# Kernel tuning notes

Hardware: AMD Instinct MI355X
Metric: run time of the kernel (lower is better)

## Reference

```python
import jax, jax.numpy as jnp
import numpy as np
from jax import lax

PATCH = 15
WIDTH_DCP = 55


def _box_sum(x, r):
    # AvgPool2d(kernel=2r+1, stride=1, padding=r, count_include_pad=True) * (2r+1)^2;
    # the kernel-size factor cancels in all mean_*/N ratios below.
    return lax.reduce_window(x, 0.0, lax.add, (1, 1, 2 * r + 1, 2 * r + 1),
                             (1, 1, 1, 1), ((0, 0), (0, 0), (r, r), (r, r)))


def _guided_filter(I, p, r, eps):
    Nn = _box_sum(jnp.ones_like(p), r)
    mean_I = _box_sum(I, r) / Nn
    mean_p = _box_sum(p, r) / Nn
    mean_Ip = _box_sum(I * p, r) / Nn
    cov_Ip = mean_Ip - mean_I * mean_p
    mean_II = _box_sum(I * I, r) / Nn
    var_I = mean_II - mean_I * mean_I
    a = cov_Ip / (var_I + eps)
    b = mean_p - a * mean_I
    mean_a = _box_sum(a, r) / Nn
    mean_b = _box_sum(b, r) / Nn
    return mean_a * I + mean_b


def _dark_channel(x):
    d = x.min(axis=1, keepdims=True)
    pad = WIDTH_DCP // 2
    d = jnp.pad(d, ((0, 0), (0, 0), (pad, pad), (pad, pad)), constant_values=1.0)
    return lax.reduce_window(d, jnp.inf, lax.min, (1, 1, WIDTH_DCP, WIDTH_DCP),
                             (1, 1, 1, 1), 'VALID')


def _map_A(x):
    N, C, H, W = x.shape
    dc = _dark_channel(x).reshape(N, -1)
    k = int(H * W * 0.001)
    _, idx = lax.top_k(dc, k)  # brightest dark-channel pixels
    xr = x.reshape(N, 3, -1)
    searched = jnp.take_along_axis(xr, jnp.broadcast_to(idx[:, None, :], (N, 3, k)), axis=2)
    A = searched.mean(axis=2)
    return jnp.broadcast_to(A[:, :, None, None], x.shape)


def _t_bccr(haze, mapA, ps):
    t1 = (mapA - haze) / (mapA - 20.0 / 255.0)
    t2 = (mapA - haze) / (mapA - 300.0 / 255.0)
    t = jnp.maximum(t1, t2).max(axis=1, keepdims=True)
    pad = ps // 2
    t = jnp.pad(t, ((0, 0), (0, 0), (pad, pad), (pad, pad)), constant_values=0.0)
    t = lax.reduce_window(t, -jnp.inf, lax.max, (1, 1, ps, ps), (1, 1, 1, 1), 'VALID')
    return jnp.clip(t, 0.05, 1.0)


def _pad_reshape(data, ps):
    N, C, H, W = data.shape
    pad_H = (ps - H % ps) % ps
    pad_W = (ps - W % ps) % ps
    padded = jnp.pad(data, ((0, 0), (0, 0), (pad_H // 2, pad_H - pad_H // 2),
                            (pad_W // 2, pad_W - pad_W // 2)), mode='edge')
    nH = padded.shape[2] // ps
    nW = padded.shape[3] // ps
    p = padded[:, 0].reshape(N, nH, ps, nW, ps).transpose(0, 1, 3, 2, 4)
    p = p.reshape(N, nH * nW, ps * ps).transpose(0, 2, 1)  # [N, ps*ps, P]
    return p, pad_H // 2, pad_W // 2, nH, nW


def _transmission(S, V1, ps, pixel_number=10, slp_length=0.1):
    X, sH, sW, nH, nW = _pad_reshape(V1, ps)  # [N, pp, P]
    Y, _, _, _, _ = _pad_reshape(S, ps)
    dX = X[:, :, None, :] - X[:, None, :, :]          # [N, pp, pp, P]
    dY = Y[:, :, None, :] - Y[:, None, :, :]
    slope = dY / (dX + 1e-8)
    smask = ((slope > -1) & (slope < 0)).astype(X.dtype)
    scount = smask.sum(axis=2)                         # [N, pp, P]
    pmask = (scount >= 0.5 * ps * ps).astype(X.dtype)
    pcount = pmask.sum(axis=1, keepdims=True)          # [N, 1, P]
    mx = (X * pmask).sum(axis=1, keepdims=True) / (pcount + 1e-5)
    my = (Y * pmask).sum(axis=1, keepdims=True) / (pcount + 1e-5)
    k = ((X * Y * pmask).sum(axis=1, keepdims=True) - pcount * mx * my) / (
        ((X * pmask) ** 2).sum(axis=1, keepdims=True) - pcount * mx ** 2 + 1e-5)
    b = my - k * mx
    t = 1.0 + k / (b + 1e-8)
    length = (1.0 + k ** 2) ** 0.5 * ((X * pmask).max(axis=1, keepdims=True)
                                      - (X + 1e8 * (1.0 - pmask)).min(axis=1, keepdims=True))
    tmask = ((pcount > pixel_number) & (length > slp_length) & (k > -1) & (k < 0)
             & (t > 0.01) & (t < 1 - 0.01)).astype(X.dtype)
    t = (t * tmask).reshape(-1, 1, nH, nW)
    t = jnp.repeat(jnp.repeat(t, ps, axis=2), ps, axis=3)  # nearest upsample x ps
    return t[:, :, sH:S.shape[2] + sH, sW:S.shape[3] + sW]


def _percentile(t, bili=0.05):
    N = t.shape[0]
    flat = jnp.where(t > 0, t, 10.0).reshape(N, -1)
    s = jnp.sort(flat, axis=1)
    n = flat.shape[1]
    idx = min(int(bili * n), n - 1)
    return s[:, idx].reshape(-1, 1, 1, 1)


def _restore(image, ps=PATCH):
    mapA = _map_A(image)
    norm = image / mapA
    mx = norm.max(axis=1, keepdims=True)
    S = 1.0 - norm.min(axis=1, keepdims=True) / (mx + 1e-8)
    V1 = 1.0 / (mx + 1e-8)
    t1 = _transmission(S, V1, ps)
    half = ps // 2
    t2 = _transmission(S[:, :, half:, half:], V1[:, :, half:, half:], ps)
    t2 = jnp.pad(t2, ((0, 0), (0, 0), (half, 0), (half, 0)), constant_values=0.0)
    t_slp = jnp.where((t1 != 0) & (t2 != 0), (t1 + t2) / 2.0,
                      jnp.where(t1 != 0, t1, t2))
    t_bl = _t_bccr(image, mapA, ps)
    t_min = _percentile(t_slp)
    t_fusion = jnp.clip(jnp.where(t_slp > 0, t_slp, t_bl), t_min, 1.0)
    t_ref = _guided_filter(image.mean(axis=1, keepdims=True), t_fusion, 2 * ps, 1e-3)
    return (image - mapA) / t_ref + mapA


def setup_inputs() -> dict:
    key = jax.random.key(0)
    image = jax.random.uniform(key, (1, 3, 480, 480), dtype=jnp.float32)
    return {"image": image}


def reference(image):
    return _restore(image)
```

## Files before the change

kernel.cpp:

```cpp
#include <hip/hip_runtime.h>
#include <math.h>

#define W 480
#define HT 480
#define HW (W*HT)
#define GE (HW/256)
#define PP 225
#define NPATCH 1024
#define EQCAP 8192

struct State {
  unsigned histA[4][256];
  unsigned slotP[4];
  unsigned slotK[4];
  float sumA[3];
  unsigned eqCount;
  float A[3];
  unsigned tminbits;
  unsigned eqIdx[EQCAP];
  float tp1[NPATCH];
  float tp2[NPATCH];
};

__device__ __forceinline__ void resolve_level(const unsigned* __restrict__ h,
                                              unsigned k_in, int desc,
                                              unsigned* lds,
                                              unsigned& chosen, unsigned& k_out) {
  int t = threadIdx.x;
  unsigned c = h[desc ? (255 - t) : t];
  lds[t] = c;
  __syncthreads();
  for (int s = 1; s < 256; s <<= 1) {
    unsigned add = (t >= s) ? lds[t - s] : 0u;
    __syncthreads();
    lds[t] += add;
    __syncthreads();
  }
  unsigned incl = lds[t];
  unsigned excl = incl - c;
  if (incl >= k_in && excl < k_in) { lds[256] = (unsigned)t; lds[257] = k_in - excl; }
  __syncthreads();
  unsigned tt = lds[256];
  k_out = lds[257];
  chosen = desc ? (255u - tt) : tt;
  __syncthreads();
}

__global__ __launch_bounds__(512) void k_rowmin(const float* __restrict__ img,
                                                float* __restrict__ rowmin, State* st) {
  __shared__ float l[534];
  int y = blockIdx.x, t = threadIdx.x;
  for (int i = t; i < 534; i += 512) {
    int col = i - 27;
    float v = 1.0f;
    if ((unsigned)col < (unsigned)W) {
      int q = y * W + col;
      v = fminf(fminf(img[q], img[HW + q]), img[2 * HW + q]);
    }
    l[i] = v;
  }
  if (y == 0 && t < 256) {
    for (int i = 0; i < 4; ++i) st->histA[i][t] = 0u;
    if (t == 0) { st->sumA[0] = 0.f; st->sumA[1] = 0.f; st->sumA[2] = 0.f; st->eqCount = 0u; }
  }
  __syncthreads();
  if (t < W) {
    float m = l[t];
    for (int d = 1; d < 55; ++d) m = fminf(m, l[t + d]);
    rowmin[y * W + t] = m;
  }
}

__global__ __launch_bounds__(256) void k_vchunk(const float* __restrict__ rowmin,
                                                float* __restrict__ cmin) {
  int p = blockIdx.x * 256 + threadIdx.x;
  if (p >= 60 * W) return;
  int c = p / W, x = p - c * W;
  float m = INFINITY;
  for (int r = 0; r < 8; ++r) m = fminf(m, rowmin[(c * 8 + r) * W + x]);
  cmin[p] = m;
}

__global__ __launch_bounds__(256) void k_minV2(const float* __restrict__ rowmin,
                                               const float* __restrict__ cmin,
                                               float* __restrict__ dc, State* st) {
  __shared__ unsigned lh[256];
  int t = threadIdx.x;
  lh[t] = 0u;
  __syncthreads();
  int p = blockIdx.x * 256 + t;
  int y = p / W, x = p - y * W;
  int lo = y - 27, hi = y + 27;
  float m = (lo < 0 || hi >= HT) ? 1.0f : INFINITY;
  int lo2 = max(lo, 0), hi2 = min(hi, HT - 1);
  int cs = (lo2 + 7) >> 3, ce = ((hi2 + 1) >> 3) - 1;
  for (int c = cs; c <= ce; ++c) m = fminf(m, cmin[c * W + x]);
  for (int yy = lo2; yy < (cs << 3); ++yy) m = fminf(m, rowmin[yy * W + x]);
  for (int yy = (ce + 1) << 3; yy <= hi2; ++yy) m = fminf(m, rowmin[yy * W + x]);
  dc[p] = m;
  atomicAdd(&lh[__float_as_uint(m) >> 24], 1u);
  __syncthreads();
  unsigned c = lh[t];
  if (c) atomicAdd(&st->histA[0][t], c);
}

__global__ __launch_bounds__(256) void k_hist(const float* __restrict__ dc,
                                              State* st, int level) {
  __shared__ unsigned lds[258];
  int t = threadIdx.x;
  unsigned prefix, k;
  if (level == 1) { prefix = 0u; k = 230u; }
  else { prefix = st->slotP[level - 2]; k = st->slotK[level - 2]; }
  unsigned ch, kn;
  resolve_level(st->histA[level - 1], k, 1, lds, ch, kn);
  prefix |= ch << (32 - 8 * level);
  k = kn;
  if (t == 0) { st->slotP[level - 1] = prefix; st->slotK[level - 1] = k; }
  __syncthreads();
  lds[t] = 0u;
  __syncthreads();
  int p = blockIdx.x * 256 + t;
  unsigned bits = __float_as_uint(dc[p]);
  unsigned mask = 0xFFFFFFFFu << (32 - 8 * level);
  if ((bits & mask) == prefix)
    atomicAdd(&lds[(bits >> (24 - 8 * level)) & 0xFFu], 1u);
  __syncthreads();
  unsigned c = lds[t];
  if (c) atomicAdd(&st->histA[level][t], c);
}

__global__ __launch_bounds__(256) void k_gatherA(const float* __restrict__ dc,
                                                 const float* __restrict__ img, State* st) {
  __shared__ unsigned lds[258];
  int t = threadIdx.x;
  unsigned prefix = st->slotP[2], k = st->slotK[2];
  unsigned ch, kn;
  resolve_level(st->histA[3], k, 1, lds, ch, kn);
  unsigned vb = prefix | ch;
  if (t == 0) { st->slotP[3] = vb; st->slotK[3] = kn; }
  int p = blockIdx.x * 256 + t;
  unsigned bits = __float_as_uint(dc[p]);
  if (bits > vb) {
    atomicAdd(&st->sumA[0], img[p]);
    atomicAdd(&st->sumA[1], img[HW + p]);
    atomicAdd(&st->sumA[2], img[2 * HW + p]);
  } else if (bits == vb) {
    unsigned pos = atomicAdd(&st->eqCount, 1u);
    if (pos < (unsigned)EQCAP) st->eqIdx[pos] = (unsigned)p;
  }
}

__global__ __launch_bounds__(256) void k_finalizeA(const float* __restrict__ img, State* st) {
  __shared__ unsigned lds[258];
  __shared__ unsigned lh[256];
  __shared__ unsigned sIdx[EQCAP];
  __shared__ float ssum[3];
  int t = threadIdx.x;
  unsigned keq = st->slotK[3];
  unsigned ne = st->eqCount; if (ne > (unsigned)EQCAP) ne = EQCAP;
  for (int i = t; i < (int)ne; i += 256) sIdx[i] = st->eqIdx[i];
  if (t < 3) ssum[t] = 0.f;
  __syncthreads();
  unsigned pfx = 0u, k = keq;
  for (int lev = 0; lev < 3; ++lev) {
    int s = 16 - 8 * lev;
    lh[t] = 0u;
    __syncthreads();
    for (int i = t; i < (int)ne; i += 256) {
      unsigned v = sIdx[i];
      if ((v >> (s + 8)) == (pfx >> (s + 8)))
        atomicAdd(&lh[(v >> s) & 0xFFu], 1u);
    }
    __syncthreads();
    unsigned ch, kn;
    resolve_level(lh, k, 0, lds, ch, kn);
    pfx |= ch << s;
    k = kn;
  }
  float a0 = 0.f, a1 = 0.f, a2 = 0.f;
  for (int i = t; i < (int)ne; i += 256) {
    unsigned q = sIdx[i];
    if (q <= pfx) { a0 += img[q]; a1 += img[HW + q]; a2 += img[2 * HW + q]; }
  }
  atomicAdd(&ssum[0], a0); atomicAdd(&ssum[1], a1); atomicAdd(&ssum[2], a2);
  __syncthreads();
  if (t == 0) {
    st->A[0] = (st->sumA[0] + ssum[0]) / 230.0f;
    st->A[1] = (st->sumA[1] + ssum[1]) / 230.0f;
    st->A[2] = (st->sumA[2] + ssum[2]) / 230.0f;
  }
}

__global__ __launch_bounds__(256) void k_elem1(const float* __restrict__ img,
                                               const State* __restrict__ st,
                                               float2* __restrict__ SV,
                                               float* __restrict__ Io, float* __restrict__ To) {
  int p = blockIdx.x * 256 + threadIdx.x;
  float A0 = st->A[0], A1 = st->A[1], A2 = st->A[2];
  float r = img[p], g = img[HW + p], bl = img[2 * HW + p];
  float nr = r / A0, ng = g / A1, nb = bl / A2;
  float mx = fmaxf(fmaxf(nr, ng), nb);
  float mn = fminf(fminf(nr, ng), nb);
  float d = mx + 1e-8f;
  float S = 1.0f - mn / d;
  float V = 1.0f / d;
  SV[p] = make_float2(V, S);
  Io[p] = ((r + g) + bl) / 3.0f;
  const float c20 = (float)(20.0 / 255.0);
  const float c300 = (float)(300.0 / 255.0);
  float t0 = fmaxf((A0 - r) / (A0 - c20), (A0 - r) / (A0 - c300));
  float t1 = fmaxf((A1 - g) / (A1 - c20), (A1 - g) / (A1 - c300));
  float t2 = fmaxf((A2 - bl) / (A2 - c20), (A2 - bl) / (A2 - c300));
  To[p] = fmaxf(fmaxf(t0, t1), t2);
}

__device__ __forceinline__ float wred_sum(float v) { for (int m = 32; m; m >>= 1) v += __shfl_xor(v, m, 64); return v; }
__device__ __forceinline__ float wred_max(float v) { for (int m = 32; m; m >>= 1) v = fmaxf(v, __shfl_xor(v, m, 64)); return v; }
__device__ __forceinline__ float wred_min(float v) { for (int m = 32; m; m >>= 1) v = fminf(v, __shfl_xor(v, m, 64)); return v; }

__global__ __launch_bounds__(256) void k_mega1(const float2* __restrict__ SV,
                                               const float* __restrict__ To,
                                               float* __restrict__ mh, State* st) {
  __shared__ float2 XY[PP];
  __shared__ float part[4][8];
  int b = blockIdx.x;
  int t = threadIdx.x;
  if (b >= 2048) {
    int p = (b - 2048) * 256 + t;
    int y = p / W, x = p - y * W;
    float m = -INFINITY;
    for (int d = -7; d <= 7; ++d) {
      int xx = x + d;
      float v = ((unsigned)xx < (unsigned)W) ? To[y * W + xx] : 0.0f;
      m = fmaxf(m, v);
    }
    mh[p] = m;
    return;
  }
  int mode = b >> 10;
  int pid = b & 1023;
  int ph = pid >> 5, pw = pid & 31;
  if (t < PP) {
    int r = t / 15, c = t - (t / 15) * 15;
    int y, x;
    if (mode == 0) { y = ph * 15 + r; x = pw * 15 + c; }
    else {
      y = ph * 15 + r + 4; y = (y < 7) ? 7 : ((y > 479) ? 479 : y);
      x = pw * 15 + c + 4; x = (x < 7) ? 7 : ((x > 479) ? 479 : x);
    }
    XY[t] = SV[y * W + x];
  }
  __syncthreads();
  float xi = 0.f, yi = 0.f;
  int cnt = 0;
  if (t < PP) {
    xi = XY[t].x; yi = XY[t].y;
    for (int j = 0; j < PP; ++j) {
      float2 o = XY[j];
      float dY = yi - o.y;
      float D = (xi - o.x) + 1e-8f;
      cnt += ((dY * D < 0.0f) && (fabsf(dY) < fabsf(D))) ? 1 : 0;
    }
  }
  float pmf = (t < PP && cnt >= 113) ? 1.0f : 0.0f;
  float xm = xi * pmf, ym = yi * pmf;
  float v0 = wred_sum(pmf);
  float v1 = wred_sum(xm);
  float v2 = wred_sum(ym);
  float v3 = wred_sum(xm * ym);
  float v4 = wred_sum(xm * xm);
  float v5 = wred_max((t < PP) ? xm : -INFINITY);
  float v6 = wred_min((t < PP) ? (xi + 1e8f * (1.0f - pmf)) : INFINITY);
  int wid = t >> 6, lane = t & 63;
  if (lane == 0) {
    part[wid][0] = v0; part[wid][1] = v1; part[wid][2] = v2; part[wid][3] = v3;
    part[wid][4] = v4; part[wid][5] = v5; part[wid][6] = v6;
  }
  __syncthreads();
  if (t == 0) {
    float pcount = 0.f, sx = 0.f, sy = 0.f, sxy = 0.f, sxx = 0.f;
    float mxX = -INFINITY, mnX = INFINITY;
    for (int w2 = 0; w2 < 4; ++w2) {
      pcount += part[w2][0]; sx += part[w2][1]; sy += part[w2][2];
      sxy += part[w2][3]; sxx += part[w2][4];
      mxX = fmaxf(mxX, part[w2][5]); mnX = fminf(mnX, part[w2][6]);
    }
    float den = pcount + 1e-5f;
    float mxv = sx / den, myv = sy / den;
    float kk = (sxy - pcount * mxv * myv) / (sxx - pcount * (mxv * mxv) + 1e-5f);
    float bb = myv - kk * mxv;
    float tt = 1.0f + kk / (bb + 1e-8f);
    float len = sqrtf(1.0f + kk * kk) * (mxX - mnX);
    bool m = (pcount > 10.0f) && (len > 0.1f) && (kk > -1.0f) && (kk < 0.0f)
             && (tt > 0.01f) && (tt < 0.99f);
    float res = tt * (m ? 1.0f : 0.0f);
    if (mode == 0) st->tp1[pid] = res; else st->tp2[pid] = res;
  }
}

__global__ __launch_bounds__(256) void k_maxV_pct(const float* __restrict__ mh,
                                                  float* __restrict__ tb, State* st) {
  __shared__ unsigned lh[256];
  __shared__ unsigned lds[258];
  __shared__ float tp1s[NPATCH], tp2s[NPATCH];
  int b = blockIdx.x;
  int t = threadIdx.x;
  if (b < GE) {
    int p = b * 256 + t;
    int y = p / W, x = p - y * W;
    float m = -INFINITY;
    for (int d = -7; d <= 7; ++d) {
      int yy = y + d;
      float v = ((unsigned)yy < (unsigned)HT) ? mh[yy * W + x] : 0.0f;
      m = fmaxf(m, v);
    }
    tb[p] = fminf(fmaxf(m, 0.05f), 1.0f);
    return;
  }
  for (int i = t; i < NPATCH; i += 256) { tp1s[i] = st->tp1[i]; tp2s[i] = st->tp2[i]; }
  __syncthreads();
  unsigned prefix = 0u, k = 11521u;
  for (int level = 0; level < 4; ++level) {
    lh[t] = 0u;
    __syncthreads();
    unsigned mask = (level == 0) ? 0u : (0xFFFFFFFFu << (32 - 8 * level));
    int shift = 24 - 8 * level;
    for (int i = t; i < NPATCH; i += 256) {
      int ph = i >> 5, pw = i & 31;
      float a = tp1s[i];
      int rcnt[2], ridx[2], ccnt[2], cidx[2];
      if (ph == 0) { rcnt[0] = 7; ridx[0] = -1; rcnt[1] = 8; ridx[1] = 0; }
      else         { rcnt[0] = 4; ridx[0] = ph - 1; rcnt[1] = 11; ridx[1] = ph; }
      if (pw == 0) { ccnt[0] = 7; cidx[0] = -1; ccnt[1] = 8; cidx[1] = 0; }
      else         { ccnt[0] = 4; cidx[0] = pw - 1; ccnt[1] = 11; cidx[1] = pw; }
      for (int ri = 0; ri < 2; ++ri)
        for (int ci = 0; ci < 2; ++ci) {
          unsigned area = (unsigned)(rcnt[ri] * ccnt[ci]);
          float bb = 0.0f;
          if (ridx[ri] >= 0 && cidx[ci] >= 0) bb = tp2s[ridx[ri] * 32 + cidx[ci]];
          float r;
          if (a != 0.0f && bb != 0.0f) r = (a + bb) / 2.0f;
          else r = (a != 0.0f) ? a : bb;
          float u = (r > 0.0f) ? r : 10.0f;
          unsigned bits = __float_as_uint(u);
          if ((bits & mask) == prefix)
            atomicAdd(&lh[(bits >> shift) & 0xFFu], area);
        }
    }
    __syncthreads();
    unsigned ch, kn;
    resolve_level(lh, k, 0, lds, ch, kn);
    prefix |= ch << shift;
    k = kn;
  }
  if (t == 0) st->tminbits = prefix;
}

__global__ __launch_bounds__(512) void k_gf1h(const float* __restrict__ I,
                                              const float* __restrict__ tb,
                                              const State* __restrict__ st,
                                              float4* __restrict__ box4) {
  __shared__ float tp1s[NPATCH], tp2s[NPATCH];
  __shared__ float Pl[540], Il[540];
  int y = blockIdx.x, t = threadIdx.x;
  for (int i = t; i < NPATCH; i += 512) { tp1s[i] = st->tp1[i]; tp2s[i] = st->tp2[i]; }
  __syncthreads();
  float tmin = __uint_as_float(st->tminbits);
  int c1row = (y / 15) * 32;
  bool c2ok = (y >= 7);
  int c2row = c2ok ? ((y - 4) / 15) * 32 : 0;
  for (int i = t; i < 540; i += 512) {
    int col = i - 30;
    float pv = 0.0f, iv = 0.0f;
    if ((unsigned)col < (unsigned)W) {
      int q = y * W + col;
      float a = tp1s[c1row + col / 15];
      float bb = 0.0f;
      if (c2ok && col >= 7) bb = tp2s[c2row + (col - 4) / 15];
      float r;
      if (a != 0.0f && bb != 0.0f) r = (a + bb) / 2.0f;
      else r = (a != 0.0f) ? a : bb;
      float v = (r > 0.0f) ? r : tb[q];
      v = (v < tmin) ? tmin : v;
      v = (v > 1.0f) ? 1.0f : v;
      pv = v; iv = I[q];
    }
    Pl[i] = pv; Il[i] = iv;
  }
  __syncthreads();
  if (t < W) {
    float sI = 0.f, sP = 0.f, sIp = 0.f, sII = 0.f;
    for (int d = 0; d < 61; ++d) {
      float iv = Il[t + d], pv = Pl[t + d];
      sI += iv; sP += pv; sIp += iv * pv; sII += iv * iv;
    }
    box4[y * W + t] = make_float4(sI, sP, sIp, sII);
  }
}

__global__ __launch_bounds__(256) void k_gf1v(const float4* __restrict__ box4,
                                              float2* __restrict__ ab) {
  int p = blockIdx.x * 256 + threadIdx.x;
  int y = p / W, x = p - y * W;
  float sI = 0.f, sP = 0.f, sIp = 0.f, sII = 0.f;
  for (int d = -30; d <= 30; ++d) {
    int yy = y + d;
    if ((unsigned)yy < (unsigned)HT) {
      float4 v = box4[yy * W + x];
      sI += v.x; sP += v.y; sIp += v.z; sII += v.w;
    }
  }
  int ny = min(y + 30, HT - 1) - max(y - 30, 0) + 1;
  int nx = min(x + 30, W - 1) - max(x - 30, 0) + 1;
  float Nn = (float)(ny * nx);
  float mI = sI / Nn, mP = sP / Nn, mIp = sIp / Nn, mII = sII / Nn;
  float cov = mIp - mI * mP;
  float var = mII - mI * mI;
  float av = cov / (var + 1e-3f);
  ab[p] = make_float2(av, mP - av * mI);
}

__global__ __launch_bounds__(512) void k_gf2h(const float2* __restrict__ ab,
                                              float2* __restrict__ hab) {
  __shared__ float2 l[540];
  int y = blockIdx.x, t = threadIdx.x;
  for (int i = t; i < 540; i += 512) {
    int col = i - 30;
    float2 v = make_float2(0.f, 0.f);
    if ((unsigned)col < (unsigned)W) v = ab[y * W + col];
    l[i] = v;
  }
  __syncthreads();
  if (t < W) {
    float sa = 0.f, sb = 0.f;
    for (int d = 0; d < 61; ++d) { float2 v = l[t + d]; sa += v.x; sb += v.y; }
    hab[y * W + t] = make_float2(sa, sb);
  }
}

__global__ __launch_bounds__(256) void k_gf2vfin(const float2* __restrict__ hab,
                                                 const float* __restrict__ I,
                                                 const float* __restrict__ img,
                                                 const State* __restrict__ st,
                                                 float* __restrict__ out) {
  int p = blockIdx.x * 256 + threadIdx.x;
  int y = p / W, x = p - y * W;
  float sa = 0.f, sb = 0.f;
  for (int d = -30; d <= 30; ++d) {
    int yy = y + d;
    if ((unsigned)yy < (unsigned)HT) { float2 v = hab[yy * W + x]; sa += v.x; sb += v.y; }
  }
  int ny = min(y + 30, HT - 1) - max(y - 30, 0) + 1;
  int nx = min(x + 30, W - 1) - max(x - 30, 0) + 1;
  float Nn = (float)(ny * nx);
  float tref = (sa / Nn) * I[p] + (sb / Nn);
  float A0 = st->A[0], A1 = st->A[1], A2 = st->A[2];
  out[p]          = (img[p]          - A0) / tref + A0;
  out[HW + p]     = (img[HW + p]     - A1) / tref + A1;
  out[2 * HW + p] = (img[2 * HW + p] - A2) / tref + A2;
}

extern "C" void kernel_launch(void* const* d_in, const int* in_sizes, int n_in,
                              void* d_out, int out_size, void* d_ws, size_t ws_size,
                              hipStream_t stream) {
  (void)in_sizes; (void)n_in; (void)out_size; (void)ws_size;
  const float* img = (const float*)d_in[0];
  float* out = (float*)d_out;
  State* st = (State*)d_ws;
  float* sb = (float*)((char*)d_ws + 65536);
  float* bufA = sb;
  float* bufB = sb + HW;
  float* bufD = sb + 2 * HW;
  float* bufF = sb + 3 * HW;
  float2* SV   = (float2*)bufF;
  float* cmin  = bufF + 2 * HW;
  float* mh    = bufF + 3 * HW;
  float4* box4 = (float4*)bufF;
  float2* hab  = (float2*)bufF;
  float2* ab   = (float2*)(sb + 7 * HW);

  dim3 b256(256), b512(512);
  dim3 ge(GE), rows(HT);

  k_rowmin<<<rows, b512, 0, stream>>>(img, bufB, st);
  k_vchunk<<<dim3(113), b256, 0, stream>>>(bufB, cmin);
  k_minV2<<<ge, b256, 0, stream>>>(bufB, cmin, bufA, st);
  for (int l = 1; l < 4; ++l)
    k_hist<<<ge, b256, 0, stream>>>(bufA, st, l);
  k_gatherA<<<ge, b256, 0, stream>>>(bufA, img, st);
  k_finalizeA<<<dim3(1), b256, 0, stream>>>(img, st);
  k_elem1<<<ge, b256, 0, stream>>>(img, st, SV, bufD, bufB);
  k_mega1<<<dim3(2048 + GE), b256, 0, stream>>>(SV, bufB, mh, st);
  k_maxV_pct<<<dim3(GE + 1), b256, 0, stream>>>(mh, bufA, st);
  k_gf1h<<<rows, b512, 0, stream>>>(bufD, bufA, st, box4);
  k_gf1v<<<ge, b256, 0, stream>>>(box4, ab);
  k_gf2h<<<rows, b512, 0, stream>>>(ab, hab);
  k_gf2vfin<<<ge, b256, 0, stream>>>(hab, bufD, img, st, out);
}
```

Baseline: 192.0 us.

## Collapse top-k radix passes into 16-bit histogram and fuse elementwise stages

Replaces the four-pass 8-bit radix select for the dark-channel top-k with one global 65536-bin histogram built in the min-filter kernel. A single-block resolve reads it, and the low 16 bits are refined inside the finalize kernel. The separate elementwise kernel is removed: S/V, the BCCR bound and the gray intensity are recomputed from the image wherever they are consumed. The guided filter's vertical pass is merged with the second horizontal pass. Together these cut about six launches and several full-image intermediate buffers. The cost is global atomics contending on the big histogram, redundant recomputation, and a plain 55-row vertical min in place of the chunked one.

Result: slower. 372.3 us (+94.0%).

```diff
diff --git a/kernel.cpp b/kernel.cpp
--- a/kernel.cpp
+++ b/kernel.cpp
@@ -10,7 +10,6 @@
 #define EQCAP 8192
 
 struct State {
-  unsigned histA[4][256];
   unsigned slotP[4];
   unsigned slotK[4];
   float sumA[3];
@@ -47,9 +46,12 @@
 }
 
 __global__ __launch_bounds__(512) void k_rowmin(const float* __restrict__ img,
-                                                float* __restrict__ rowmin, State* st) {
+                                                float* __restrict__ rowmin,
+                                                State* st, unsigned* __restrict__ hist16) {
   __shared__ float l[534];
   int y = blockIdx.x, t = threadIdx.x;
+  int g = y * 512 + t;
+  if (g < 65536) hist16[g] = 0u;
   for (int i = t; i < 534; i += 512) {
     int col = i - 27;
     float v = 1.0f;
@@ -59,10 +61,7 @@
     }
     l[i] = v;
   }
-  if (y == 0 && t < 256) {
-    for (int i = 0; i < 4; ++i) st->histA[i][t] = 0u;
-    if (t == 0) { st->sumA[0] = 0.f; st->sumA[1] = 0.f; st->sumA[2] = 0.f; st->eqCount = 0u; }
-  }
+  if (g == 0) { st->sumA[0] = 0.f; st->sumA[1] = 0.f; st->sumA[2] = 0.f; st->eqCount = 0u; }
   __syncthreads();
   if (t < W) {
     float m = l[t];
@@ -71,105 +70,99 @@
   }
 }
 
-__global__ __launch_bounds__(256) void k_vchunk(const float* __restrict__ rowmin,
-                                                float* __restrict__ cmin) {
-  int p = blockIdx.x * 256 + threadIdx.x;
-  if (p >= 60 * W) return;
-  int c = p / W, x = p - c * W;
-  float m = INFINITY;
-  for (int r = 0; r < 8; ++r) m = fminf(m, rowmin[(c * 8 + r) * W + x]);
-  cmin[p] = m;
-}
-
-__global__ __launch_bounds__(256) void k_minV2(const float* __restrict__ rowmin,
-                                               const float* __restrict__ cmin,
-                                               float* __restrict__ dc, State* st) {
-  __shared__ unsigned lh[256];
-  int t = threadIdx.x;
-  lh[t] = 0u;
-  __syncthreads();
+__global__ __launch_bounds__(256) void k_minV3(const float* __restrict__ rowmin,
+                                               float* __restrict__ dc,
+                                               unsigned* __restrict__ hist16) {
+  int t = threadIdx.x;
   int p = blockIdx.x * 256 + t;
   int y = p / W, x = p - y * W;
   int lo = y - 27, hi = y + 27;
   float m = (lo < 0 || hi >= HT) ? 1.0f : INFINITY;
   int lo2 = max(lo, 0), hi2 = min(hi, HT - 1);
-  int cs = (lo2 + 7) >> 3, ce = ((hi2 + 1) >> 3) - 1;
-  for (int c = cs; c <= ce; ++c) m = fminf(m, cmin[c * W + x]);
-  for (int yy = lo2; yy < (cs << 3); ++yy) m = fminf(m, rowmin[yy * W + x]);
-  for (int yy = (ce + 1) << 3; yy <= hi2; ++yy) m = fminf(m, rowmin[yy * W + x]);
+  for (int yy = lo2; yy <= hi2; ++yy) m = fminf(m, rowmin[yy * W + x]);
   dc[p] = m;
-  atomicAdd(&lh[__float_as_uint(m) >> 24], 1u);
-  __syncthreads();
-  unsigned c = lh[t];
-  if (c) atomicAdd(&st->histA[0][t], c);
-}
-
-__global__ __launch_bounds__(256) void k_hist(const float* __restrict__ dc,
-                                              State* st, int level) {
+  atomicAdd(&hist16[__float_as_uint(m) >> 16], 1u);
+}
+
+__global__ __launch_bounds__(256) void k_resolve16(const unsigned* __restrict__ hist16,
+                                                   State* st) {
   __shared__ unsigned lds[258];
-  int t = threadIdx.x;
-  unsigned prefix, k;
-  if (level == 1) { prefix = 0u; k = 230u; }
-  else { prefix = st->slotP[level - 2]; k = st->slotK[level - 2]; }
-  unsigned ch, kn;
-  resolve_level(st->histA[level - 1], k, 1, lds, ch, kn);
-  prefix |= ch << (32 - 8 * level);
-  k = kn;
-  if (t == 0) { st->slotP[level - 1] = prefix; st->slotK[level - 1] = k; }
-  __syncthreads();
-  lds[t] = 0u;
-  __syncthreads();
+  __shared__ unsigned lh[256];
+  int t = threadIdx.x;
+  const uint4* h4 = (const uint4*)hist16;
+  unsigned s = 0;
+  for (int i = 0; i < 64; ++i) { uint4 v = h4[t * 64 + i]; s += v.x + v.y + v.z + v.w; }
+  lh[t] = s;
+  __syncthreads();
+  unsigned ct, kc;
+  resolve_level(lh, 230u, 1, lds, ct, kc);
+  lh[t] = hist16[ct * 256 + t];
+  __syncthreads();
+  unsigned b, kp;
+  resolve_level(lh, kc, 1, lds, b, kp);
+  if (t == 0) { st->slotP[0] = (ct << 8) | b; st->slotK[0] = kp; }
+}
+
+__global__ __launch_bounds__(256) void k_gather2(const float* __restrict__ dc,
+                                                 const float* __restrict__ img, State* st) {
+  int t = threadIdx.x;
   int p = blockIdx.x * 256 + t;
-  unsigned bits = __float_as_uint(dc[p]);
-  unsigned mask = 0xFFFFFFFFu << (32 - 8 * level);
-  if ((bits & mask) == prefix)
-    atomicAdd(&lds[(bits >> (24 - 8 * level)) & 0xFFu], 1u);
-  __syncthreads();
-  unsigned c = lds[t];
-  if (c) atomicAdd(&st->histA[level][t], c);
-}
-
-__global__ __launch_bounds__(256) void k_gatherA(const float* __restrict__ dc,
-                                                 const float* __restrict__ img, State* st) {
-  __shared__ unsigned lds[258];
-  int t = threadIdx.x;
-  unsigned prefix = st->slotP[2], k = st->slotK[2];
-  unsigned ch, kn;
-  resolve_level(st->histA[3], k, 1, lds, ch, kn);
-  unsigned vb = prefix | ch;
-  if (t == 0) { st->slotP[3] = vb; st->slotK[3] = kn; }
-  int p = blockIdx.x * 256 + t;
-  unsigned bits = __float_as_uint(dc[p]);
-  if (bits > vb) {
+  unsigned p16 = st->slotP[0];
+  unsigned b16 = __float_as_uint(dc[p]) >> 16;
+  if (b16 > p16) {
     atomicAdd(&st->sumA[0], img[p]);
     atomicAdd(&st->sumA[1], img[HW + p]);
     atomicAdd(&st->sumA[2], img[2 * HW + p]);
-  } else if (bits == vb) {
+  } else if (b16 == p16) {
     unsigned pos = atomicAdd(&st->eqCount, 1u);
     if (pos < (unsigned)EQCAP) st->eqIdx[pos] = (unsigned)p;
   }
 }
 
-__global__ __launch_bounds__(256) void k_finalizeA(const float* __restrict__ img, State* st) {
+__global__ __launch_bounds__(256) void k_finalizeA2(const float* __restrict__ dc,
+                                                    const float* __restrict__ img, State* st) {
   __shared__ unsigned lds[258];
   __shared__ unsigned lh[256];
   __shared__ unsigned sIdx[EQCAP];
+  __shared__ unsigned short sVal[EQCAP];
   __shared__ float ssum[3];
   int t = threadIdx.x;
-  unsigned keq = st->slotK[3];
+  unsigned k = st->slotK[0];
   unsigned ne = st->eqCount; if (ne > (unsigned)EQCAP) ne = EQCAP;
-  for (int i = t; i < (int)ne; i += 256) sIdx[i] = st->eqIdx[i];
+  for (int i = t; i < (int)ne; i += 256) {
+    unsigned q = st->eqIdx[i];
+    sIdx[i] = q;
+    sVal[i] = (unsigned short)(__float_as_uint(dc[q]) & 0xFFFFu);
+  }
   if (t < 3) ssum[t] = 0.f;
   __syncthreads();
-  unsigned pfx = 0u, k = keq;
+  unsigned vpfx = 0u;
+  for (int lev = 0; lev < 2; ++lev) {
+    int s = 8 - 8 * lev;
+    lh[t] = 0u;
+    __syncthreads();
+    for (int i = t; i < (int)ne; i += 256) {
+      unsigned v = (unsigned)sVal[i];
+      if (lev == 0 || (v >> 8) == (vpfx >> 8))
+        atomicAdd(&lh[(v >> s) & 0xFFu], 1u);
+    }
+    __syncthreads();
+    unsigned ch, kn;
+    resolve_level(lh, k, 1, lds, ch, kn);
+    vpfx |= ch << s;
+    k = kn;
+  }
+  unsigned pfx = 0u;
   for (int lev = 0; lev < 3; ++lev) {
     int s = 16 - 8 * lev;
     lh[t] = 0u;
     __syncthreads();
     for (int i = t; i < (int)ne; i += 256) {
-      unsigned v = sIdx[i];
-      if ((v >> (s + 8)) == (pfx >> (s + 8)))
-        atomicAdd(&lh[(v >> s) & 0xFFu], 1u);
+      if ((unsigned)sVal[i] == vpfx) {
+        unsigned v = sIdx[i];
+        if ((v >> (s + 8)) == (pfx >> (s + 8)))
+          atomicAdd(&lh[(v >> s) & 0xFFu], 1u);
+      }
     }
     __syncthreads();
     unsigned ch, kn;
@@ -179,8 +172,10 @@
   }
   float a0 = 0.f, a1 = 0.f, a2 = 0.f;
   for (int i = t; i < (int)ne; i += 256) {
-    unsigned q = sIdx[i];
-    if (q <= pfx) { a0 += img[q]; a1 += img[HW + q]; a2 += img[2 * HW + q]; }
+    unsigned v = (unsigned)sVal[i], q = sIdx[i];
+    if (v > vpfx || (v == vpfx && q <= pfx)) {
+      a0 += img[q]; a1 += img[HW + q]; a2 += img[2 * HW + q];
+    }
   }
   atomicAdd(&ssum[0], a0); atomicAdd(&ssum[1], a1); atomicAdd(&ssum[2], a2);
   __syncthreads();
@@ -191,50 +186,41 @@
   }
 }
 
-__global__ __launch_bounds__(256) void k_elem1(const float* __restrict__ img,
-                                               const State* __restrict__ st,
-                                               float2* __restrict__ SV,
-                                               float* __restrict__ Io, float* __restrict__ To) {
-  int p = blockIdx.x * 256 + threadIdx.x;
-  float A0 = st->A[0], A1 = st->A[1], A2 = st->A[2];
-  float r = img[p], g = img[HW + p], bl = img[2 * HW + p];
-  float nr = r / A0, ng = g / A1, nb = bl / A2;
-  float mx = fmaxf(fmaxf(nr, ng), nb);
-  float mn = fminf(fminf(nr, ng), nb);
-  float d = mx + 1e-8f;
-  float S = 1.0f - mn / d;
-  float V = 1.0f / d;
-  SV[p] = make_float2(V, S);
-  Io[p] = ((r + g) + bl) / 3.0f;
-  const float c20 = (float)(20.0 / 255.0);
-  const float c300 = (float)(300.0 / 255.0);
-  float t0 = fmaxf((A0 - r) / (A0 - c20), (A0 - r) / (A0 - c300));
-  float t1 = fmaxf((A1 - g) / (A1 - c20), (A1 - g) / (A1 - c300));
-  float t2 = fmaxf((A2 - bl) / (A2 - c20), (A2 - bl) / (A2 - c300));
-  To[p] = fmaxf(fmaxf(t0, t1), t2);
-}
-
 __device__ __forceinline__ float wred_sum(float v) { for (int m = 32; m; m >>= 1) v += __shfl_xor(v, m, 64); return v; }
 __device__ __forceinline__ float wred_max(float v) { for (int m = 32; m; m >>= 1) v = fmaxf(v, __shfl_xor(v, m, 64)); return v; }
 __device__ __forceinline__ float wred_min(float v) { for (int m = 32; m; m >>= 1) v = fminf(v, __shfl_xor(v, m, 64)); return v; }
 
-__global__ __launch_bounds__(256) void k_mega1(const float2* __restrict__ SV,
-                                               const float* __restrict__ To,
+__global__ __launch_bounds__(256) void k_mega1(const float* __restrict__ img,
                                                float* __restrict__ mh, State* st) {
   __shared__ float2 XY[PP];
   __shared__ float part[4][8];
+  __shared__ float Tl[494];
   int b = blockIdx.x;
   int t = threadIdx.x;
+  float A0 = st->A[0], A1 = st->A[1], A2 = st->A[2];
+  const float c20 = (float)(20.0 / 255.0);
+  const float c300 = (float)(300.0 / 255.0);
   if (b >= 2048) {
-    int p = (b - 2048) * 256 + t;
-    int y = p / W, x = p - y * W;
-    float m = -INFINITY;
-    for (int d = -7; d <= 7; ++d) {
-      int xx = x + d;
-      float v = ((unsigned)xx < (unsigned)W) ? To[y * W + xx] : 0.0f;
-      m = fmaxf(m, v);
-    }
-    mh[p] = m;
+    int y = b - 2048;
+    for (int i = t; i < 494; i += 256) {
+      int col = i - 7;
+      float v = 0.0f;
+      if ((unsigned)col < (unsigned)W) {
+        int q = y * W + col;
+        float r = img[q], g = img[HW + q], bl = img[2 * HW + q];
+        float t0 = fmaxf((A0 - r) / (A0 - c20), (A0 - r) / (A0 - c300));
+        float t1 = fmaxf((A1 - g) / (A1 - c20), (A1 - g) / (A1 - c300));
+        float t2 = fmaxf((A2 - bl) / (A2 - c20), (A2 - bl) / (A2 - c300));
+        v = fmaxf(fmaxf(t0, t1), t2);
+      }
+      Tl[i] = v;
+    }
+    __syncthreads();
+    for (int x = t; x < W; x += 256) {
+      float m = -INFINITY;
+      for (int d = 0; d < 15; ++d) m = fmaxf(m, Tl[x + d]);
+      mh[y * W + x] = m;
+    }
     return;
   }
   int mode = b >> 10;
@@ -248,13 +234,20 @@
       y = ph * 15 + r + 4; y = (y < 7) ? 7 : ((y > 479) ? 479 : y);
       x = pw * 15 + c + 4; x = (x < 7) ? 7 : ((x > 479) ? 479 : x);
     }
-    XY[t] = SV[y * W + x];
+    int q = y * W + x;
+    float rr = img[q], gg = img[HW + q], bb = img[2 * HW + q];
+    float nr = rr / A0, ng = gg / A1, nb = bb / A2;
+    float mx = fmaxf(fmaxf(nr, ng), nb);
+    float mn = fminf(fminf(nr, ng), nb);
+    float d = mx + 1e-8f;
+    XY[t] = make_float2(1.0f / d, 1.0f - mn / d);
   }
   __syncthreads();
   float xi = 0.f, yi = 0.f;
   int cnt = 0;
   if (t < PP) {
     xi = XY[t].x; yi = XY[t].y;
+    #pragma unroll 5
     for (int j = 0; j < PP; ++j) {
       float2 o = XY[j];
       float dY = yi - o.y;
@@ -356,7 +349,7 @@
   if (t == 0) st->tminbits = prefix;
 }
 
-__global__ __launch_bounds__(512) void k_gf1h(const float* __restrict__ I,
+__global__ __launch_bounds__(512) void k_gf1h(const float* __restrict__ img,
                                               const float* __restrict__ tb,
                                               const State* __restrict__ st,
                                               float4* __restrict__ box4) {
@@ -383,7 +376,8 @@
       float v = (r > 0.0f) ? r : tb[q];
       v = (v < tmin) ? tmin : v;
       v = (v > 1.0f) ? 1.0f : v;
-      pv = v; iv = I[q];
+      pv = v;
+      iv = ((img[q] + img[HW + q]) + img[2 * HW + q]) / 3.0f;
     }
     Pl[i] = pv; Il[i] = iv;
   }
@@ -398,48 +392,40 @@
   }
 }
 
-__global__ __launch_bounds__(256) void k_gf1v(const float4* __restrict__ box4,
-                                              float2* __restrict__ ab) {
-  int p = blockIdx.x * 256 + threadIdx.x;
-  int y = p / W, x = p - y * W;
-  float sI = 0.f, sP = 0.f, sIp = 0.f, sII = 0.f;
-  for (int d = -30; d <= 30; ++d) {
-    int yy = y + d;
-    if ((unsigned)yy < (unsigned)HT) {
-      float4 v = box4[yy * W + x];
-      sI += v.x; sP += v.y; sIp += v.z; sII += v.w;
-    }
-  }
-  int ny = min(y + 30, HT - 1) - max(y - 30, 0) + 1;
-  int nx = min(x + 30, W - 1) - max(x - 30, 0) + 1;
-  float Nn = (float)(ny * nx);
-  float mI = sI / Nn, mP = sP / Nn, mIp = sIp / Nn, mII = sII / Nn;
-  float cov = mIp - mI * mP;
-  float var = mII - mI * mI;
-  float av = cov / (var + 1e-3f);
-  ab[p] = make_float2(av, mP - av * mI);
-}
-
-__global__ __launch_bounds__(512) void k_gf2h(const float2* __restrict__ ab,
-                                              float2* __restrict__ hab) {
+__global__ __launch_bounds__(512) void k_gf1vh(const float4* __restrict__ box4,
+                                               float2* __restrict__ hab) {
   __shared__ float2 l[540];
   int y = blockIdx.x, t = threadIdx.x;
-  for (int i = t; i < 540; i += 512) {
-    int col = i - 30;
-    float2 v = make_float2(0.f, 0.f);
-    if ((unsigned)col < (unsigned)W) v = ab[y * W + col];
-    l[i] = v;
-  }
+  float2 v = make_float2(0.f, 0.f);
+  if (t < W) {
+    float sI = 0.f, sP = 0.f, sIp = 0.f, sII = 0.f;
+    for (int d = -30; d <= 30; ++d) {
+      int yy = y + d;
+      if ((unsigned)yy < (unsigned)HT) {
+        float4 b = box4[yy * W + t];
+        sI += b.x; sP += b.y; sIp += b.z; sII += b.w;
+      }
+    }
+    int ny = min(y + 30, HT - 1) - max(y - 30, 0) + 1;
+    int nx = min(t + 30, W - 1) - max(t - 30, 0) + 1;
+    float Nn = (float)(ny * nx);
+    float mI = sI / Nn, mP = sP / Nn, mIp = sIp / Nn, mII = sII / Nn;
+    float cov = mIp - mI * mP;
+    float var = mII - mI * mI;
+    float av = cov / (var + 1e-3f);
+    v = make_float2(av, mP - av * mI);
+  }
+  if (t < 30) { l[t] = make_float2(0.f, 0.f); l[510 + t] = make_float2(0.f, 0.f); }
+  if (t < W) l[30 + t] = v;
   __syncthreads();
   if (t < W) {
     float sa = 0.f, sb = 0.f;
-    for (int d = 0; d < 61; ++d) { float2 v = l[t + d]; sa += v.x; sb += v.y; }
+    for (int d = 0; d < 61; ++d) { float2 u = l[t + d]; sa += u.x; sb += u.y; }
     hab[y * W + t] = make_float2(sa, sb);
   }
 }
 
 __global__ __launch_bounds__(256) void k_gf2vfin(const float2* __restrict__ hab,
-                                                 const float* __restrict__ I,
                                                  const float* __restrict__ img,
                                                  const State* __restrict__ st,
                                                  float* __restrict__ out) {
@@ -453,11 +439,13 @@
   int ny = min(y + 30, HT - 1) - max(y - 30, 0) + 1;
   int nx = min(x + 30, W - 1) - max(x - 30, 0) + 1;
   float Nn = (float)(ny * nx);
-  float tref = (sa / Nn) * I[p] + (sb / Nn);
+  float r = img[p], g = img[HW + p], bl = img[2 * HW + p];
+  float Iv = ((r + g) + bl) / 3.0f;
+  float tref = (sa / Nn) * Iv + (sb / Nn);
   float A0 = st->A[0], A1 = st->A[1], A2 = st->A[2];
-  out[p]          = (img[p]          - A0) / tref + A0;
-  out[HW + p]     = (img[HW + p]     - A1) / tref + A1;
-  out[2 * HW + p] = (img[2 * HW + p] - A2) / tref + A2;
+  out[p]          = (r  - A0) / tref + A0;
+  out[HW + p]     = (g  - A1) / tref + A1;
+  out[2 * HW + p] = (bl - A2) / tref + A2;
 }
 
 extern "C" void kernel_launch(void* const* d_in, const int* in_sizes, int n_in,
@@ -467,33 +455,24 @@
   const float* img = (const float*)d_in[0];
   float* out = (float*)d_out;
   State* st = (State*)d_ws;
-  float* sb = (float*)((char*)d_ws + 65536);
+  unsigned* hist16 = (unsigned*)((char*)d_ws + 65536);
+  float* sb = (float*)((char*)d_ws + 65536 + 262144);
   float* bufA = sb;
   float* bufB = sb + HW;
-  float* bufD = sb + 2 * HW;
-  float* bufF = sb + 3 * HW;
-  float2* SV   = (float2*)bufF;
-  float* cmin  = bufF + 2 * HW;
-  float* mh    = bufF + 3 * HW;
-  float4* box4 = (float4*)bufF;
-  float2* hab  = (float2*)bufF;
-  float2* ab   = (float2*)(sb + 7 * HW);
+  float4* box4 = (float4*)(sb + 2 * HW);
+  float2* hab  = (float2*)(sb + 6 * HW);
 
   dim3 b256(256), b512(512);
   dim3 ge(GE), rows(HT);
 
-  k_rowmin<<<rows, b512, 0, stream>>>(img, bufB, st);
-  k_vchunk<<<dim3(113), b256, 0, stream>>>(bufB, cmin);
-  k_minV2<<<ge, b256, 0, stream>>>(bufB, cmin, bufA, st);
-  for (int l = 1; l < 4; ++l)
-    k_hist<<<ge, b256, 0, stream>>>(bufA, st, l);
-  k_gatherA<<<ge, b256, 0, stream>>>(bufA, img, st);
-  k_finalizeA<<<dim3(1), b256, 0, stream>>>(img, st);
-  k_elem1<<<ge, b256, 0, stream>>>(img, st, SV, bufD, bufB);
-  k_mega1<<<dim3(2048 + GE), b256, 0, stream>>>(SV, bufB, mh, st);
-  k_maxV_pct<<<dim3(GE + 1), b256, 0, stream>>>(mh, bufA, st);
-  k_gf1h<<<rows, b512, 0, stream>>>(bufD, bufA, st, box4);
-  k_gf1v<<<ge, b256, 0, stream>>>(box4, ab);
-  k_gf2h<<<rows, b512, 0, stream>>>(ab, hab);
-  k_gf2vfin<<<ge, b256, 0, stream>>>(hab, bufD, img, st, out);
-}
+  k_rowmin<<<rows, b512, 0, stream>>>(img, bufB, st, hist16);
+  k_minV3<<<ge, b256, 0, stream>>>(bufB, bufA, hist16);
+  k_resolve16<<<dim3(1), b256, 0, stream>>>(hist16, st);
+  k_gather2<<<ge, b256, 0, stream>>>(bufA, img, st);
+  k_finalizeA2<<<dim3(1), b256, 0, stream>>>(bufA, img, st);
+  k_mega1<<<dim3(2048 + HT), b256, 0, stream>>>(img, bufB, st);
+  k_maxV_pct<<<dim3(GE + 1), b256, 0, stream>>>(bufB, bufA, st);
+  k_gf1h<<<rows, b512, 0, stream>>>(img, bufA, st, box4);
+  k_gf1vh<<<rows, b512, 0, stream>>>(box4, hab);
+  k_gf2vfin<<<ge, b256, 0, stream>>>(hab, img, st, out);
+}
```
